# Optimization experiments

Measured on AMD Instinct MI355X. Metric: run time of the kernel, lower is better.

## Reference

```python
import jax, jax.numpy as jnp
import numpy as np

DIM = 192
WS = (7, 7, 7)
NUM_HEADS = 6
N = WS[0] * WS[1] * WS[2]  # 343
HEAD_DIM = DIM // NUM_HEADS
SCALE = HEAD_DIM ** -0.5
TABLE_SIZE = (2 * WS[0] - 1) * (2 * WS[1] - 1) * (2 * WS[2] - 1)  # 2197


def _relative_position_index():
    coords = np.stack(np.meshgrid(np.arange(WS[0]), np.arange(WS[1]), np.arange(WS[2])))
    cf = coords.reshape(3, -1)  # [3, N]
    rel = cf[:, :, None] - cf[:, None, :]  # [3, N, N]
    rel = rel.transpose(1, 2, 0)
    rel[:, :, 0] += WS[0] - 1
    rel[:, :, 1] += WS[1] - 1
    rel[:, :, 2] += WS[2] - 1
    rel[:, :, 0] *= (2 * WS[1] - 1) * (2 * WS[2] - 1)
    rel[:, :, 1] *= 2 * WS[2] - 1
    return rel.sum(-1)  # [N, N] int


_RPI = jnp.asarray(_relative_position_index())


def setup_inputs() -> dict:
    key = jax.random.key(0)
    ks = jax.random.split(key, 6)
    B = 256
    x = jax.random.normal(ks[0], (B, N, DIM), dtype=jnp.float32)
    mask = jax.random.normal(ks[1], (64, N, N), dtype=jnp.float32)
    qkv_w = jax.random.normal(ks[2], (DIM, 3 * DIM), dtype=jnp.float32) * (DIM ** -0.5)
    rpb_table = jax.random.normal(ks[3], (TABLE_SIZE, NUM_HEADS), dtype=jnp.float32) * 0.02
    proj_w = jax.random.normal(ks[4], (DIM, DIM), dtype=jnp.float32) * (DIM ** -0.5)
    proj_b = jax.random.normal(ks[5], (DIM,), dtype=jnp.float32) * 0.01
    return {"x": x, "mask": mask, "qkv_w": qkv_w, "rpb_table": rpb_table,
            "proj_w": proj_w, "proj_b": proj_b}


def reference(x, mask, qkv_w, rpb_table, proj_w, proj_b):
    b, n, c = x.shape
    h = NUM_HEADS
    # qkv projection (no bias), split into q,k,v of shape [b, h, n, hd]
    qkv = (x @ qkv_w).reshape(b, n, 3, h, c // h).transpose(2, 0, 3, 1, 4)
    q, k, v = qkv[0], qkv[1], qkv[2]
    q = q * SCALE
    attn = jnp.einsum('bhqd,bhkd->bhqk', q, k)  # [b, h, n, n]
    # gathered relative position bias: [n, n, h] -> [h, n, n]
    bias = rpb_table[_RPI[:n, :n].reshape(-1)].reshape(n, n, h)
    attn = attn + jnp.transpose(bias, (2, 0, 1))[None]
    nw = mask.shape[0]
    nwww = max(b // nw, 1)
    attn = attn.reshape(nwww, nw, h, n, n) + mask[None, :, None]
    attn = attn.reshape(-1, h, n, n)
    attn = jax.nn.softmax(attn, axis=-1)
    out = jnp.einsum('bhqk,bhkd->bhqd', attn, v)
    out = jnp.swapaxes(out, 1, 2).reshape(b, n, c)
    return out @ proj_w + proj_b
```

## Files before the change

### kernel.cpp

```cpp
#include <hip/hip_runtime.h>

typedef __attribute__((ext_vector_type(8))) short bf16x8;
typedef __attribute__((ext_vector_type(4))) float f32x4;
typedef __attribute__((ext_vector_type(4))) int i32x4;

#define MFMA16(a,b,c) __builtin_amdgcn_mfma_f32_16x16x32_bf16(a,b,c,0,0,0)

#define SCALE 0.1767766952966369f

static __device__ __forceinline__ f32x4 zero4(){
    f32x4 z = {0.f,0.f,0.f,0.f};
    return z;
}

static __device__ __forceinline__ float bf2f(unsigned short u){
    unsigned int x = ((unsigned int)u) << 16;
    return __builtin_bit_cast(float, x);
}
static __device__ __forceinline__ unsigned short f2bf(float f){
    __bf16 b = (__bf16)f;
    return __builtin_bit_cast(unsigned short, b);
}

__global__ __launch_bounds__(256) void k_prep_wt(const float* __restrict__ qkv_w,
                                                 unsigned short* __restrict__ wt){
    int i = blockIdx.x*256 + threadIdx.x;
    if (i < 576*192){ int n = i/192, kk = i%192; wt[i] = f2bf(qkv_w[kk*576 + n]); }
}
__global__ __launch_bounds__(256) void k_prep_pwt(const float* __restrict__ proj_w,
                                                  unsigned short* __restrict__ pwt){
    int i = blockIdx.x*256 + threadIdx.x;
    if (i < 192*192){ int n = i/192, kk = i%192; pwt[i] = f2bf(proj_w[kk*192 + n]); }
}
__global__ __launch_bounds__(256) void k_prep_bias(const float* __restrict__ rpb,
                                                   unsigned short* __restrict__ bias){
    int i = blockIdx.x*256 + threadIdx.x;
    if (i >= 6*343*352) return;
    int h = i / (343*352); int rem = i % (343*352);
    int qi = rem / 352, ci = rem % 352;
    unsigned short v = 0;
    if (ci < 343){
        int qa=qi/49, qr=qi%49, qb=qr/7, qc=qr%7;
        int ka=ci/49, kr=ci%49, kb=kr/7, kc=kr%7;
        int idx = 169*(qb-kb+6) + 13*(qa-ka+6) + (qc-kc+6);
        v = f2bf(rpb[idx*6 + h]);
    }
    bias[i] = v;
}

__global__ __launch_bounds__(256) void k_qkv(const float* __restrict__ x,
                                             const unsigned short* __restrict__ wt,
                                             unsigned short* __restrict__ q,
                                             unsigned short* __restrict__ k,
                                             unsigned short* __restrict__ vt){
    __shared__ __attribute__((aligned(16))) unsigned short Bs[576*40];
    const int tid  = threadIdx.x;
    const int wid  = tid>>6, lane = tid&63, quad = lane>>4, l15 = lane&15;
    const int m0   = blockIdx.x*64;
    f32x4 acc[36];
    #pragma unroll
    for (int st=0; st<36; ++st) acc[st] = zero4();
    const float* arow = x + (m0 + wid*16 + l15)*192 + quad*8;
    for (int k0=0; k0<192; k0+=32){
        __syncthreads();
        for (int i=tid; i<2304; i+=256){
            int rr=i>>2, cc=(i&3)<<3;
            *(i32x4*)&Bs[rr*40+cc] = *(const i32x4*)(wt + rr*192 + k0 + cc);
        }
        __syncthreads();
        f32x4 af0 = *(const f32x4*)(arow + k0);
        f32x4 af1 = *(const f32x4*)(arow + k0 + 4);
        bf16x8 a;
        #pragma unroll
        for (int j=0; j<4; ++j){
            a[j]   = (short)f2bf(af0[j]);
            a[4+j] = (short)f2bf(af1[j]);
        }
        #pragma unroll
        for (int st=0; st<36; ++st){
            bf16x8 b = *(const bf16x8*)&Bs[(st*16+l15)*40 + quad*8];
            acc[st] = MFMA16(a, b, acc[st]);
        }
    }
    #pragma unroll
    for (int r=0; r<4; ++r){
        int tm = m0 + wid*16 + quad*4 + r;
        int bb = tm/343, tt = tm%343;
        #pragma unroll
        for (int st=0; st<36; ++st){
            const int f0 = st*16;
            const int s  = f0/192, h = (f0%192)>>5, d0 = f0&31;
            int d = d0 + l15;
            float v = acc[st][r];
            if (s==0)      q[((bb*6+h)*343 + tt)*32 + d] = f2bf(v*SCALE);
            else if (s==1) k[((bb*6+h)*343 + tt)*32 + d] = f2bf(v);
            else           vt[((bb*6+h)*32 + d)*344 + tt] = f2bf(v);
        }
    }
}

__global__ __launch_bounds__(256) void k_attn(const unsigned short* __restrict__ q,
                                              const unsigned short* __restrict__ kg,
                                              const unsigned short* __restrict__ vt,
                                              const float* __restrict__ mask,
                                              const unsigned short* __restrict__ bias,
                                              unsigned short* __restrict__ ao){
    __shared__ __attribute__((aligned(16))) unsigned short Ks[352*40];
    __shared__ __attribute__((aligned(16))) unsigned short Vs[32*344 + 64];
    __shared__ __attribute__((aligned(16))) unsigned short Pb[4*2*640];
    const int tid = threadIdx.x;
    const int wid = tid>>6, lane = tid&63, quad = lane>>4, l15 = lane&15;
    const int idx = blockIdx.x;
    const int w = idx/24, sub = idx%24, g = sub/6, h = sub%6, b = g*64 + w;
    const int bh = b*6 + h;
    const unsigned short* kb  = kg + bh*10976;
    const unsigned short* vb  = vt + bh*11008;
    const unsigned short* qb  = q  + bh*10976;
    const float*          mw  = mask + w*117649;
    const unsigned short* bhp = bias + h*120736;

    for (int i=tid; i<1372; i+=256){
        int rr=i>>2, cc=(i&3)<<3;
        *(i32x4*)&Ks[rr*40+cc] = *(const i32x4*)(kb + rr*32 + cc);
    }
    for (int i=tid; i<1376; i+=256)
        *(i32x4*)&Vs[i*8] = *(const i32x4*)(vb + i*8);
    if (tid < 64) Vs[32*344 + tid] = 0;
    __syncthreads();

    for (int chunk=wid; chunk<22; chunk+=4){
        int qrow = chunk*16 + l15; if (qrow > 342) qrow = 342;
        bf16x8 a = *(const bf16x8*)(qb + qrow*32 + quad*8);
        f32x4 s[22];
        #pragma unroll
        for (int t=0; t<22; ++t){
            bf16x8 bb = *(const bf16x8*)&Ks[(t*16+l15)*40 + quad*8];
            s[t] = MFMA16(a, bb, zero4());
        }
        const int row0 = chunk*16 + quad*4;
        #pragma unroll
        for (int r=0; r<4; ++r){
            int row = row0 + r; int rowc = row>342 ? 342 : row;
            const float*          mrow = mw  + rowc*343;
            const unsigned short* brow = bhp + rowc*352;
            #pragma unroll
            for (int t=0; t<22; ++t){
                int col  = t*16 + l15;
                int colc = col>342 ? 342 : col;
                s[t][r] += mrow[colc] + bf2f(brow[col]);
            }
        }
        if (l15 >= 7){
            #pragma unroll
            for (int r=0; r<4; ++r) s[21][r] = -1e30f;
        }
        f32x4 mx, sm, inv;
        #pragma unroll
        for (int r=0; r<4; ++r){
            float m = s[0][r];
            #pragma unroll
            for (int t=1; t<22; ++t) m = fmaxf(m, s[t][r]);
            mx[r] = m;
        }
        #pragma unroll
        for (int d=1; d<16; d<<=1){
            #pragma unroll
            for (int r=0; r<4; ++r) mx[r] = fmaxf(mx[r], __shfl_xor(mx[r], d));
        }
        #pragma unroll
        for (int r=0; r<4; ++r){
            float acc = 0.f;
            #pragma unroll
            for (int t=0; t<22; ++t){ float e = __expf(s[t][r]-mx[r]); s[t][r]=e; acc += e; }
            sm[r] = acc;
        }
        #pragma unroll
        for (int d=1; d<16; d<<=1){
            #pragma unroll
            for (int r=0; r<4; ++r) sm[r] += __shfl_xor(sm[r], d);
        }
        #pragma unroll
        for (int r=0; r<4; ++r) inv[r] = 1.0f / sm[r];

        f32x4 o0 = zero4(), o1 = zero4();
        unsigned short* pw0 = Pb + wid*1280;
        #pragma unroll
        for (int ks=0; ks<11; ++ks){
            unsigned short* pw = pw0 + (ks&1)*640;
            #pragma unroll
            for (int tt=0; tt<2; ++tt){
                int t = ks*2+tt;
                #pragma unroll
                for (int r=0; r<4; ++r)
                    pw[(quad*4+r)*40 + tt*16 + l15] = f2bf(s[t][r]*inv[r]);
            }
            asm volatile("s_waitcnt lgkmcnt(0)" ::: "memory");
            bf16x8 ap = *(const bf16x8*)&pw[l15*40 + quad*8];
            bf16x8 v0 = *(const bf16x8*)&Vs[l15*344      + ks*32 + quad*8];
            bf16x8 v1 = *(const bf16x8*)&Vs[(16+l15)*344 + ks*32 + quad*8];
            o0 = MFMA16(ap, v0, o0);
            o1 = MFMA16(ap, v1, o1);
        }
        #pragma unroll
        for (int r=0; r<4; ++r){
            int nt = row0 + r;
            if (nt < 343){
                unsigned short* dst = ao + (b*343 + nt)*192 + h*32;
                dst[l15]    = f2bf(o0[r]);
                dst[16+l15] = f2bf(o1[r]);
            }
        }
    }
}

__global__ __launch_bounds__(256) void k_proj(const unsigned short* __restrict__ ao,
                                              const unsigned short* __restrict__ pwt,
                                              const float* __restrict__ pbias,
                                              float* __restrict__ out){
    const int tid = threadIdx.x, wid = tid>>6, lane = tid&63, quad = lane>>4, l15 = lane&15;
    const int m0 = blockIdx.x*64 + wid*16;
    f32x4 acc[12];
    #pragma unroll
    for (int st=0; st<12; ++st) acc[st] = zero4();
    float bl[12];
    #pragma unroll
    for (int st=0; st<12; ++st) bl[st] = pbias[st*16 + l15];
    const unsigned short* arow = ao + (m0 + l15)*192 + quad*8;
    for (int k0=0; k0<192; k0+=32){
        bf16x8 a = *(const bf16x8*)(arow + k0);
        #pragma unroll
        for (int st=0; st<12; ++st){
            bf16x8 bb = *(const bf16x8*)(pwt + (st*16+l15)*192 + k0 + quad*8);
            acc[st] = MFMA16(a, bb, acc[st]);
        }
    }
    #pragma unroll
    for (int r=0; r<4; ++r){
        int tm = m0 + quad*4 + r;
        #pragma unroll
        for (int st=0; st<12; ++st)
            out[tm*192 + st*16 + l15] = acc[st][r] + bl[st];
    }
}

extern "C" void kernel_launch(void* const* d_in, const int* in_sizes, int n_in,
                              void* d_out, int out_size, void* d_ws, size_t ws_size,
                              hipStream_t stream){
    const float* x     = (const float*)d_in[0];
    const float* mask  = (const float*)d_in[1];
    const float* qkv_w = (const float*)d_in[2];
    const float* rpb   = (const float*)d_in[3];
    const float* projw = (const float*)d_in[4];
    const float* projb = (const float*)d_in[5];
    float* out = (float*)d_out;
    unsigned short* ws  = (unsigned short*)d_ws;

    unsigned short* wt   = ws;
    unsigned short* pwt  = wt   + 110592;
    unsigned short* bias = pwt  + 36864;
    unsigned short* q    = bias + 724416;
    unsigned short* k    = q    + 16859136;
    unsigned short* vt   = k    + 16859136;
    unsigned short* ao   = vt   + 16908288;

    hipLaunchKernelGGL(k_prep_wt,   dim3(432),  dim3(256), 0, stream, qkv_w, wt);
    hipLaunchKernelGGL(k_prep_pwt,  dim3(144),  dim3(256), 0, stream, projw, pwt);
    hipLaunchKernelGGL(k_prep_bias, dim3(2830), dim3(256), 0, stream, rpb, bias);
    hipLaunchKernelGGL(k_qkv,       dim3(1372), dim3(256), 0, stream, x, wt, q, k, vt);
    hipLaunchKernelGGL(k_attn,      dim3(1536), dim3(256), 0, stream, q, k, vt, mask, bias, ao);
    hipLaunchKernelGGL(k_proj,      dim3(1372), dim3(256), 0, stream, ao, pwt, projb, out);
}
```

Before: 524.9 us.

## Retile QKV GEMM into N-split blocks with double-buffered weights; transpose V in attention

The QKV projection kernel now gives each block one of q/k/v (192 output columns) over 128 rows. It uses a double-buffered LDS weight tile with register prefetch of the next k-slice, a single LDS barrier per step, and a 3-blocks-per-CU launch bound. V is now stored token-major, which makes its writes coalesced like q and k, and the attention kernel transposes V into LDS itself. This is meant to cut register pressure, shorten the barrier stalls, and remove the strided transposed global stores, at the cost of re-reading x three times and doing scattered 2-byte LDS writes in attention.

```diff
diff --git a/kernel.cpp b/kernel.cpp
--- a/kernel.cpp
+++ b/kernel.cpp
@@ -12,7 +12,6 @@
     f32x4 z = {0.f,0.f,0.f,0.f};
     return z;
 }
-
 static __device__ __forceinline__ float bf2f(unsigned short u){
     unsigned int x = ((unsigned int)u) << 16;
     return __builtin_bit_cast(float, x);
@@ -20,6 +19,10 @@
 static __device__ __forceinline__ unsigned short f2bf(float f){
     __bf16 b = (__bf16)f;
     return __builtin_bit_cast(unsigned short, b);
+}
+static __device__ __forceinline__ void bar_lds(){
+    asm volatile("s_waitcnt lgkmcnt(0)" ::: "memory");
+    __builtin_amdgcn_s_barrier();
 }
 
 __global__ __launch_bounds__(256) void k_prep_wt(const float* __restrict__ qkv_w,
@@ -48,60 +51,89 @@
     bias[i] = v;
 }
 
-__global__ __launch_bounds__(256) void k_qkv(const float* __restrict__ x,
-                                             const unsigned short* __restrict__ wt,
-                                             unsigned short* __restrict__ q,
-                                             unsigned short* __restrict__ k,
-                                             unsigned short* __restrict__ vt){
-    __shared__ __attribute__((aligned(16))) unsigned short Bs[576*40];
-    const int tid  = threadIdx.x;
-    const int wid  = tid>>6, lane = tid&63, quad = lane>>4, l15 = lane&15;
-    const int m0   = blockIdx.x*64;
-    f32x4 acc[36];
-    #pragma unroll
-    for (int st=0; st<36; ++st) acc[st] = zero4();
-    const float* arow = x + (m0 + wid*16 + l15)*192 + quad*8;
-    for (int k0=0; k0<192; k0+=32){
-        __syncthreads();
-        for (int i=tid; i<2304; i+=256){
-            int rr=i>>2, cc=(i&3)<<3;
-            *(i32x4*)&Bs[rr*40+cc] = *(const i32x4*)(wt + rr*192 + k0 + cc);
-        }
-        __syncthreads();
-        f32x4 af0 = *(const f32x4*)(arow + k0);
-        f32x4 af1 = *(const f32x4*)(arow + k0 + 4);
-        bf16x8 a;
-        #pragma unroll
-        for (int j=0; j<4; ++j){
-            a[j]   = (short)f2bf(af0[j]);
-            a[4+j] = (short)f2bf(af1[j]);
-        }
-        #pragma unroll
-        for (int st=0; st<36; ++st){
-            bf16x8 b = *(const bf16x8*)&Bs[(st*16+l15)*40 + quad*8];
-            acc[st] = MFMA16(a, b, acc[st]);
-        }
-    }
-    #pragma unroll
-    for (int r=0; r<4; ++r){
-        int tm = m0 + wid*16 + quad*4 + r;
-        int bb = tm/343, tt = tm%343;
-        #pragma unroll
-        for (int st=0; st<36; ++st){
-            const int f0 = st*16;
-            const int s  = f0/192, h = (f0%192)>>5, d0 = f0&31;
-            int d = d0 + l15;
-            float v = acc[st][r];
-            if (s==0)      q[((bb*6+h)*343 + tt)*32 + d] = f2bf(v*SCALE);
-            else if (s==1) k[((bb*6+h)*343 + tt)*32 + d] = f2bf(v);
-            else           vt[((bb*6+h)*32 + d)*344 + tt] = f2bf(v);
+__global__ __launch_bounds__(256, 3) void k_qkv(const float* __restrict__ x,
+                                                const unsigned short* __restrict__ wt,
+                                                unsigned short* __restrict__ q,
+                                                unsigned short* __restrict__ k,
+                                                unsigned short* __restrict__ v){
+    __shared__ __attribute__((aligned(16))) unsigned short Bs[2][192*40];
+    const int tid = threadIdx.x;
+    const int wid = tid>>6, lane = tid&63, quad = lane>>4, l15 = lane&15;
+    const int nq = blockIdx.x % 3;
+    const int mg = blockIdx.x / 3;
+    const int srr = tid>>2, scc = (tid&3)<<3;
+
+    f32x4 acc[24];
+    #pragma unroll
+    for (int i=0;i<24;++i) acc[i] = zero4();
+
+    const unsigned short* wtb = wt + nq*192*192;
+    i32x4 s0, s1, s2;
+    s0 = *(const i32x4*)(wtb + (srr      )*192 + scc);
+    s1 = *(const i32x4*)(wtb + (srr +  64)*192 + scc);
+    s2 = *(const i32x4*)(wtb + (srr + 128)*192 + scc);
+
+    const int r0 = mg*128 + wid*32 + l15;
+    const float* xp0 = x + (long)r0*192 + quad*8;
+    const float* xp1 = xp0 + 16*192;
+    f32x4 xa0 = *(const f32x4*)(xp0);
+    f32x4 xa1 = *(const f32x4*)(xp0+4);
+    f32x4 xb0 = *(const f32x4*)(xp1);
+    f32x4 xb1 = *(const f32x4*)(xp1+4);
+
+    for (int k0=0; k0<6; ++k0){
+        unsigned short* B = &Bs[k0&1][0];
+        *(i32x4*)&B[(srr      )*40 + scc] = s0;
+        *(i32x4*)&B[(srr +  64)*40 + scc] = s1;
+        *(i32x4*)&B[(srr + 128)*40 + scc] = s2;
+        if (k0 < 5){
+            const unsigned short* wn = wtb + (k0+1)*32;
+            s0 = *(const i32x4*)(wn + (srr      )*192 + scc);
+            s1 = *(const i32x4*)(wn + (srr +  64)*192 + scc);
+            s2 = *(const i32x4*)(wn + (srr + 128)*192 + scc);
+        }
+        bf16x8 a0, a1;
+        #pragma unroll
+        for (int j=0;j<4;++j){
+            a0[j] = (short)f2bf(xa0[j]); a0[4+j] = (short)f2bf(xa1[j]);
+            a1[j] = (short)f2bf(xb0[j]); a1[4+j] = (short)f2bf(xb1[j]);
+        }
+        if (k0 < 5){
+            xa0 = *(const f32x4*)(xp0 + (k0+1)*32);
+            xa1 = *(const f32x4*)(xp0 + (k0+1)*32 + 4);
+            xb0 = *(const f32x4*)(xp1 + (k0+1)*32);
+            xb1 = *(const f32x4*)(xp1 + (k0+1)*32 + 4);
+        }
+        bar_lds();
+        #pragma unroll
+        for (int nt=0; nt<12; ++nt){
+            bf16x8 b = *(const bf16x8*)&B[(nt*16+l15)*40 + quad*8];
+            acc[nt]    = MFMA16(a0, b, acc[nt]);
+            acc[12+nt] = MFMA16(a1, b, acc[12+nt]);
+        }
+    }
+
+    unsigned short* dst = (nq==0) ? q : (nq==1) ? k : v;
+    const float mul = (nq==0) ? SCALE : 1.0f;
+    #pragma unroll
+    for (int mt=0; mt<2; ++mt){
+        #pragma unroll
+        for (int r=0; r<4; ++r){
+            int tm = mg*128 + wid*32 + mt*16 + quad*4 + r;
+            int bb = tm/343, tt = tm%343;
+            #pragma unroll
+            for (int nt=0; nt<12; ++nt){
+                int cc = nt*16 + l15;
+                int h = cc>>5, d = cc&31;
+                dst[((bb*6+h)*343 + tt)*32 + d] = f2bf(acc[mt*12+nt][r]*mul);
+            }
         }
     }
 }
 
 __global__ __launch_bounds__(256) void k_attn(const unsigned short* __restrict__ q,
                                               const unsigned short* __restrict__ kg,
-                                              const unsigned short* __restrict__ vt,
+                                              const unsigned short* __restrict__ vg,
                                               const float* __restrict__ mask,
                                               const unsigned short* __restrict__ bias,
                                               unsigned short* __restrict__ ao){
@@ -114,7 +146,7 @@
     const int w = idx/24, sub = idx%24, g = sub/6, h = sub%6, b = g*64 + w;
     const int bh = b*6 + h;
     const unsigned short* kb  = kg + bh*10976;
-    const unsigned short* vb  = vt + bh*11008;
+    const unsigned short* vb  = vg + bh*10976;
     const unsigned short* qb  = q  + bh*10976;
     const float*          mw  = mask + w*117649;
     const unsigned short* bhp = bias + h*120736;
@@ -123,8 +155,13 @@
         int rr=i>>2, cc=(i&3)<<3;
         *(i32x4*)&Ks[rr*40+cc] = *(const i32x4*)(kb + rr*32 + cc);
     }
-    for (int i=tid; i<1376; i+=256)
-        *(i32x4*)&Vs[i*8] = *(const i32x4*)(vb + i*8);
+    for (int i=tid; i<1372; i+=256){
+        int tok=i>>2, c=(i&3)<<3;
+        bf16x8 vv = *(const bf16x8*)(vb + tok*32 + c);
+        #pragma unroll
+        for (int j=0;j<8;++j) Vs[(c+j)*344 + tok] = (unsigned short)vv[j];
+    }
+    if (tid < 32) Vs[tid*344 + 343] = 0;
     if (tid < 64) Vs[32*344 + tid] = 0;
     __syncthreads();
 
@@ -260,13 +297,13 @@
     unsigned short* bias = pwt  + 36864;
     unsigned short* q    = bias + 724416;
     unsigned short* k    = q    + 16859136;
-    unsigned short* vt   = k    + 16859136;
-    unsigned short* ao   = vt   + 16908288;
+    unsigned short* v    = k    + 16859136;
+    unsigned short* ao   = v    + 16859136;
 
     hipLaunchKernelGGL(k_prep_wt,   dim3(432),  dim3(256), 0, stream, qkv_w, wt);
     hipLaunchKernelGGL(k_prep_pwt,  dim3(144),  dim3(256), 0, stream, projw, pwt);
     hipLaunchKernelGGL(k_prep_bias, dim3(2830), dim3(256), 0, stream, rpb, bias);
-    hipLaunchKernelGGL(k_qkv,       dim3(1372), dim3(256), 0, stream, x, wt, q, k, vt);
-    hipLaunchKernelGGL(k_attn,      dim3(1536), dim3(256), 0, stream, q, k, vt, mask, bias, ao);
+    hipLaunchKernelGGL(k_qkv,       dim3(2058), dim3(256), 0, stream, x, wt, q, k, v);
+    hipLaunchKernelGGL(k_attn,      dim3(1536), dim3(256), 0, stream, q, k, v, mask, bias, ao);
     hipLaunchKernelGGL(k_proj,      dim3(1372), dim3(256), 0, stream, ao, pwt, projb, out);
 }
```

Result: faster. 459.5 us (-12.5%).
